# Optimization experiments

Hardware: AMD Instinct MI355X
Metric: run time of the kernel (lower is better)

Reference implementation:

```python
import jax, jax.numpy as jnp
import numpy as np

B, T, C, NH = 2, 128, 384, 6
H = 768          # memory MLP hidden (expansion=2)
P, M = 4, 16     # persistent + long-term memory tokens; prefix_len = P+M
LR, MOM, DECAY = 0.01, 0.9, 0.001

def setup_inputs() -> dict:
    key = jax.random.key(0)
    ks = jax.random.split(key, 12)
    s = 0.02
    return {
        'x':          jax.random.normal(ks[0], (B, T, C), jnp.float32),
        'c_attn_w':   jax.random.normal(ks[1], (C, 3 * C), jnp.float32) * s,
        'c_attn_b':   jnp.zeros((3 * C,), jnp.float32),
        'c_proj_w':   jax.random.normal(ks[2], (C, C), jnp.float32) * s,
        'c_proj_b':   jnp.zeros((C,), jnp.float32),
        'ln1_g': jnp.ones((C,), jnp.float32), 'ln1_b': jnp.zeros((C,), jnp.float32),
        'ln2_g': jnp.ones((C,), jnp.float32), 'ln2_b': jnp.zeros((C,), jnp.float32),
        'fc_w':       jax.random.normal(ks[3], (C, 4 * C), jnp.float32) * s,
        'fc_b':       jnp.zeros((4 * C,), jnp.float32),
        'pr_w':       jax.random.normal(ks[4], (4 * C, C), jnp.float32) * s,
        'pr_b':       jnp.zeros((C,), jnp.float32),
        'mem_w1':     jax.random.normal(ks[5], (C, H), jnp.float32) * s,
        'mem_w2':     jax.random.normal(ks[6], (H, C), jnp.float32) * s,
        'wk':         jax.random.normal(ks[7], (C, C), jnp.float32) * s,
        'wv':         jax.random.normal(ks[8], (C, C), jnp.float32) * s,
        'mem_queries': jax.random.normal(ks[9], (M, C), jnp.float32) * s,
        'persist':    jax.random.normal(ks[10], (P, C), jnp.float32) * s,
    }

def _ln(x, g, b):
    mu = jnp.mean(x, -1, keepdims=True)
    var = jnp.mean((x - mu) ** 2, -1, keepdims=True)
    return (x - mu) * jax.lax.rsqrt(var + 1e-5) * g + b

def _scan_log(gates, tokens):
    # x[t] = gate[t]*x[t-1] + token[t] via log-cumsum trick (scan axis = 1)
    while gates.ndim < tokens.ndim:
        gates = gates[..., None]
    g = jnp.clip(gates, 1e-7, 1.0 - 1e-7)
    lc = jnp.cumsum(jnp.log(g), axis=1)
    return jnp.cumsum(tokens * jnp.exp(-lc), axis=1) * jnp.exp(lc)

def _forward(x, c_attn_w, c_attn_b, c_proj_w, c_proj_b, ln1_g, ln1_b, ln2_g, ln2_b,
             fc_w, fc_b, pr_w, pr_b, mem_w1, mem_w2, wk, wv, mem_queries, persist):
    b = x.shape[0]
    hd = C // NH
    PL = P + M
    xn = _ln(x, ln1_g, ln1_b)
    # --- retrieve long-term memory tokens with previous-segment memory weights ---
    retr = jax.nn.silu(mem_queries @ mem_w1) @ mem_w2              # [M, C]
    pref = jnp.concatenate([persist, retr], axis=0)                # [PL, C]
    seq = jnp.concatenate([jnp.broadcast_to(pref, (b, PL, C)), xn], axis=1)  # [b, t, C]
    t = seq.shape[1]
    # --- prefix-LM masked attention ---
    qkv = seq @ c_attn_w + c_attn_b
    q, k, v = jnp.split(qkv, 3, axis=-1)
    def heads(z):
        return z.reshape(b, t, NH, hd).transpose(0, 2, 1, 3)       # [b, nh, t, hd]
    q, k, v = heads(q), heads(k), heads(v)
    sc = jnp.einsum('bhqd,bhkd->bhqk', q, k) / np.float32(np.sqrt(hd))
    idx = jnp.arange(t)
    kp = idx < PL  # key in prefix
    # prefix_lm_mask: key_in_prefix OR (both in suffix AND causal)
    allowed = kp[None, :] | ((~kp[:, None]) & (~kp[None, :]) & (idx[:, None] >= idx[None, :]))
    sc = jnp.where(allowed, sc, -jnp.inf)
    y = jnp.einsum('bhqk,bhkd->bhqd', jax.nn.softmax(sc, axis=-1), v)
    y = y.transpose(0, 2, 1, 3).reshape(b, t, C) @ c_proj_w + c_proj_b
    h1 = x + y[:, PL:, :]                                          # suffix (segment) outputs
    h2n = _ln(h1, ln2_g, ln2_b)
    h2 = h1 + (jax.nn.gelu(h2n @ fc_w + fc_b) @ pr_w + pr_b)
    # --- Titans neural memory update (per-token grads + momentum/decay scans) ---
    km = xn @ wk                                                   # [b, T, C]
    vm = xn @ wv
    hh = km @ mem_w1                                               # [b, T, H]
    a = jax.nn.silu(hh)
    err = a @ mem_w2 - vm                                          # [b, T, C]
    dw2 = jnp.einsum('bth,btc->bthc', a, err)                      # [b, T, H, C]
    sg = jax.nn.sigmoid(hh)
    dh = (err @ mem_w2.T) * (sg * (1.0 + hh * (1.0 - sg)))         # silu'
    dw1 = jnp.einsum('btc,bth->btch', km, dh)                      # [b, T, C, H]
    gm = jnp.full((b, T), MOM, x.dtype)
    scale = -(LR * (1.0 - MOM))
    m1 = _scan_log(gm, scale * dw1)
    m2 = _scan_log(gm, scale * dw2)
    def upd(w0, m):  # W[t] = (1-decay)*W[t-1] + m[t], W[-1] = w0
        toks = jnp.concatenate([jnp.broadcast_to(w0, (b,) + w0.shape)[:, None], m], axis=1)
        g = jnp.concatenate([jnp.ones((b, 1), x.dtype),
                             jnp.full((b, T), 1.0 - DECAY, x.dtype)], axis=1)
        return _scan_log(g, toks)[:, -1]
    w1f = upd(mem_w1, m1)                                          # [b, C, H]
    w2f = upd(mem_w2, m2)                                          # [b, H, C]
    # --- combine block output with updated-memory retrieval ---
    mem_out = jnp.einsum('bth,bhc->btc',
                         jax.nn.silu(jnp.einsum('btc,bch->bth', h2, w1f)), w2f)
    return h2 + mem_out

def reference(x, c_attn_w, c_attn_b, c_proj_w, c_proj_b, ln1_g, ln1_b, ln2_g, ln2_b,
              fc_w, fc_b, pr_w, pr_b, mem_w1, mem_w2, wk, wv, mem_queries, persist):
    return _forward(x, c_attn_w, c_attn_b, c_proj_w, c_proj_b, ln1_g, ln1_b, ln2_g, ln2_b,
                    fc_w, fc_b, pr_w, pr_b, mem_w1, mem_w2, wk, wv, mem_queries, persist)
```

## Files before the change

### kernel.cpp

```cpp
#include <hip/hip_runtime.h>
#include <math.h>

#define B_ 2
#define T_ 128
#define Cc 384
#define NH_ 6
#define HD 64
#define Hh 768
#define P_ 4
#define M_ 16
#define PL_ 20
#define TT 148

typedef unsigned short u16;
typedef short short8 __attribute__((ext_vector_type(8)));
typedef float f32x4 __attribute__((ext_vector_type(4)));

__device__ __forceinline__ u16 f2bf(float f) {
  unsigned int u = __float_as_uint(f);
  u += 0x7FFFu + ((u >> 16) & 1u);
  return (u16)(u >> 16);
}
__device__ __forceinline__ float siluf(float v) { return v / (1.f + expf(-v)); }
__device__ __forceinline__ float geluf(float v) {
  float x3 = v*v*v;
  return 0.5f*v*(1.f + tanhf(0.7978845608028654f*(v + 0.044715f*x3)));
}
template<int ACT> __device__ __forceinline__ float act_apply(float v) {
  if (ACT == 1) return geluf(v);
  if (ACT == 2) return siluf(v);
  return v;
}
__device__ __forceinline__ float coef_f(int k) {
  float e = (float)(T_ - k);
  return (exp2f(e * -0.00144342f) - exp2f(e * -0.15200310f)) * (1.0f/0.099f);
}
__device__ __forceinline__ void st_tr4(u16* dst, float v0, float v1, float v2, float v3) {
  union { u16 u[4]; uint2 d; } q;
  q.u[0]=f2bf(v0); q.u[1]=f2bf(v1); q.u[2]=f2bf(v2); q.u[3]=f2bf(v3);
  *(uint2*)dst = q.d;
}
__device__ __forceinline__ float wave_sum(float s) {
  #pragma unroll
  for (int off = 32; off; off >>= 1) s += __shfl_xor(s, off);
  return s;
}

struct Prm {
  const float *x,*c_attn_w,*c_attn_b,*c_proj_w,*c_proj_b,*ln1_g,*ln1_b,*ln2_g,*ln2_b,
              *fc_w,*fc_b,*pr_w,*pr_b,*mem_w1,*mem_w2,*wk,*wv,*mem_q,*persist;
  float *qkv,*vmb,*h1,*h2,*hhb,*outp;
  u16 *cattnT,*cprojT,*wkT,*wvT,*fcT,*prT,*w1tr,*w2tr,*w2pl,*memq,*hid,*seqb,*yb,*h2n,
      *fco,*h2b,*kmb,*kmTc,*ab,*abTc,*errB,*errT,*dhT,*w1fT,*w2fT,*ub;
  float scale, dpow;
};

template<int KSTEPS>
__device__ __forceinline__ void mfma_core(const u16* __restrict__ A,
    const u16* __restrict__ BT, int M, int mBase, int nBase, float (*red)[64][36])
{
  const long K = (long)KSTEPS * 128;
  int l = threadIdx.x & 63, w = threadIdx.x >> 6;
  int lr = l & 15, kg = l >> 4;
  long r0 = (long)min(mBase + lr, M - 1);
  long r1 = (long)min(mBase + 16 + lr, M - 1);
  long c0 = nBase + lr;
  long ko = (long)w * KSTEPS * 32 + kg * 8;
  const u16* pa0 = A + r0*K + ko;
  const u16* pa1 = A + r1*K + ko;
  const u16* pb0 = BT + c0*K + ko;
  const u16* pb1 = BT + (c0+16)*K + ko;
  const u16* pb2 = BT + (c0+32)*K + ko;
  const u16* pb3 = BT + (c0+48)*K + ko;
  f32x4 acc[2][4] = {};
  short8 a0 = *(const short8*)pa0, a1 = *(const short8*)pa1;
  short8 b0 = *(const short8*)pb0, b1 = *(const short8*)pb1;
  short8 b2 = *(const short8*)pb2, b3 = *(const short8*)pb3;
  #pragma unroll
  for (int t = 0; t < KSTEPS; ++t) {
    short8 xa0=a0, xa1=a1, xb0=b0, xb1=b1, xb2=b2, xb3=b3;
    if (t+1 < KSTEPS) {
      int o = (t+1)*32;
      a0 = *(const short8*)(pa0+o); a1 = *(const short8*)(pa1+o);
      b0 = *(const short8*)(pb0+o); b1 = *(const short8*)(pb1+o);
      b2 = *(const short8*)(pb2+o); b3 = *(const short8*)(pb3+o);
    }
    acc[0][0] = __builtin_amdgcn_mfma_f32_16x16x32_bf16(xa0, xb0, acc[0][0], 0,0,0);
    acc[0][1] = __builtin_amdgcn_mfma_f32_16x16x32_bf16(xa0, xb1, acc[0][1], 0,0,0);
    acc[0][2] = __builtin_amdgcn_mfma_f32_16x16x32_bf16(xa0, xb2, acc[0][2], 0,0,0);
    acc[0][3] = __builtin_amdgcn_mfma_f32_16x16x32_bf16(xa0, xb3, acc[0][3], 0,0,0);
    acc[1][0] = __builtin_amdgcn_mfma_f32_16x16x32_bf16(xa1, xb0, acc[1][0], 0,0,0);
    acc[1][1] = __builtin_amdgcn_mfma_f32_16x16x32_bf16(xa1, xb1, acc[1][1], 0,0,0);
    acc[1][2] = __builtin_amdgcn_mfma_f32_16x16x32_bf16(xa1, xb2, acc[1][2], 0,0,0);
    acc[1][3] = __builtin_amdgcn_mfma_f32_16x16x32_bf16(xa1, xb3, acc[1][3], 0,0,0);
  }
  #pragma unroll
  for (int i = 0; i < 2; ++i)
    #pragma unroll
    for (int j = 0; j < 4; ++j)
      *(f32x4*)&red[w][j*16 + lr][i*16 + kg*4] = acc[i][j];
  __syncthreads();
}

__device__ __forceinline__ void reduce8(float (*red)[64][36], float v[8], int& row0, int& col) {
  int tid = threadIdx.x;
  col = tid & 63;
  row0 = (tid >> 6) * 8;
  #pragma unroll
  for (int q = 0; q < 2; ++q) {
    f32x4 s = *(f32x4*)&red[0][col][row0 + q*4];
    s += *(f32x4*)&red[1][col][row0 + q*4];
    s += *(f32x4*)&red[2][col][row0 + q*4];
    s += *(f32x4*)&red[3][col][row0 + q*4];
    v[q*4+0] = s[0]; v[q*4+1] = s[1]; v[q*4+2] = s[2]; v[q*4+3] = s[3];
  }
}

template<int KSTEPS, int ACT, bool BIAS, bool RES, bool STF, bool STB, bool STTR>
__device__ __forceinline__ void gemm_task(const u16* A, const u16* BT,
    const float* bias, const float* res, float rscale,
    float* outF, u16* outB, u16* outT, int M, int N,
    int xx, int yy, float (*red)[64][36])
{
  int mBase = yy*32, nBase = xx*64;
  mfma_core<KSTEPS>(A, BT, M, mBase, nBase, red);
  float v[8]; int row0, col;
  reduce8(red, v, row0, col);
  int c = nBase + col;
  float bv = BIAS ? bias[c] : 0.f;
  #pragma unroll
  for (int q = 0; q < 8; ++q) {
    int r = mBase + row0 + q;
    float val = act_apply<ACT>(v[q] + bv);
    if (RES && r < M) val += rscale * res[(long)r*N + c];
    v[q] = val;
    if (r < M) {
      if (STF) outF[(long)r*N + c] = val;
      if (STB) outB[(long)r*N + c] = f2bf(val);
    }
  }
  if (STTR) {
    #pragma unroll
    for (int q = 0; q < 2; ++q) {
      int r = mBase + row0 + q*4;
      if (r < M) {
        int zz = r >> 7, t0 = r & 127;
        st_tr4(&outT[((long)zz*N + c)*128 + t0], v[q*4], v[q*4+1], v[q*4+2], v[q*4+3]);
      }
    }
  }
}

__global__ __launch_bounds__(256)
void k0_prep(Prm p)
{
  __shared__ float lds[1056];
  const int t = blockIdx.x;
  const int tid = threadIdx.x, w = tid >> 6, lane = tid & 63;
  if (t < 2592) {
    const float* src; u16* dst; int K, N, tile;
    int b = t;
    if (b < 432)       { src=p.c_attn_w; dst=p.cattnT; K=384;  N=1152; tile=b; }
    else if (b < 576)  { src=p.c_proj_w; dst=p.cprojT; K=384;  N=384;  tile=b-432; }
    else if (b < 720)  { src=p.wk;       dst=p.wkT;    K=384;  N=384;  tile=b-576; }
    else if (b < 864)  { src=p.wv;       dst=p.wvT;    K=384;  N=384;  tile=b-720; }
    else if (b < 1440) { src=p.fc_w;     dst=p.fcT;    K=384;  N=1536; tile=b-864; }
    else if (b < 2016) { src=p.pr_w;     dst=p.prT;    K=1536; N=384;  tile=b-1440; }
    else if (b < 2304) { src=p.mem_w1;   dst=p.w1tr;   K=384;  N=768;  tile=b-2016; }
    else               { src=p.mem_w2;   dst=p.w2tr;   K=768;  N=384;  tile=b-2304; }
    int ntx = N >> 5;
    int n0 = (tile % ntx) << 5, k0 = (tile / ntx) << 5;
    float (*fl)[33] = reinterpret_cast<float(*)[33]>(lds);
    int tr = tid >> 3, tc4 = (tid & 7) << 2;
    float4 vv = *(const float4*)&src[(long)(k0 + tr)*N + n0 + tc4];
    fl[tr][tc4] = vv.x; fl[tr][tc4+1] = vv.y; fl[tr][tc4+2] = vv.z; fl[tr][tc4+3] = vv.w;
    __syncthreads();
    st_tr4(&dst[(long)(n0 + tr)*K + k0 + tc4],
           fl[tc4][tr], fl[tc4+1][tr], fl[tc4+2][tr], fl[tc4+3][tr]);
  } else if (t < 2888) {
    int i = (t - 2592)*256 + tid;
    if (i < 73728) {
      float4 v = *(const float4*)&p.mem_w2[(long)i*4];
      st_tr4(&p.w2pl[(long)i*4], v.x, v.y, v.z, v.w);
    } else if (i < 73728 + 1536) {
      int j = i - 73728;
      float4 v = *(const float4*)&p.mem_q[(long)j*4];
      st_tr4(&p.memq[(long)j*4], v.x, v.y, v.z, v.w);
    } else if (i < 73728 + 1536 + 384) {
      int j = i - 73728 - 1536;
      float4 v = *(const float4*)&p.persist[(long)j*4];
      st_tr4(&p.seqb[(long)j*4], v.x, v.y, v.z, v.w);
      st_tr4(&p.seqb[(long)TT*384 + j*4], v.x, v.y, v.z, v.w);
    }
  } else {
    int row = (t - 2888)*4 + w;
    const float* src = p.x + (long)row*384;
    float v[6];
    #pragma unroll
    for (int i = 0; i < 6; ++i) v[i] = src[lane + i*64];
    float mu = wave_sum(v[0]+v[1]+v[2]+v[3]+v[4]+v[5]) * (1.f/384.f);
    float sq = 0.f;
    #pragma unroll
    for (int i = 0; i < 6; ++i) { float d = v[i]-mu; sq += d*d; }
    float rstd = rsqrtf(wave_sum(sq)*(1.f/384.f) + 1e-5f);
    u16* dst = p.seqb + ((long)(row >> 7)*TT + PL_ + (row & 127))*384;
    #pragma unroll
    for (int i = 0; i < 6; ++i) {
      int cc = lane + i*64;
      dst[cc] = f2bf((v[i]-mu)*rstd*p.ln1_g[cc] + p.ln1_b[cc]);
    }
  }
}

__global__ __launch_bounds__(256, 2)
void k0b_hid(Prm p)
{
  __shared__ float red[4][64][36];
  gemm_task<3,2,false,false,false,true,false>(p.memq, p.w1tr, nullptr, nullptr, 0.f,
      nullptr, p.hid, nullptr, 16, 768, blockIdx.x, 0, red);
}

__global__ __launch_bounds__(256, 2)
void k0c_retr(Prm p)
{
  __shared__ float red[4][64][36];
  int nBase = blockIdx.x*64;
  mfma_core<6>(p.hid, p.w2tr, 16, 0, nBase, red);
  float v[8]; int row0, col;
  reduce8(red, v, row0, col);
  int c = nBase + col;
  #pragma unroll
  for (int q = 0; q < 8; ++q) {
    int r = row0 + q;
    if (r < 16) {
      u16 bv = f2bf(v[q]);
      p.seqb[(long)(P_ + r)*384 + c] = bv;
      p.seqb[(long)(TT + P_ + r)*384 + c] = bv;
    }
  }
}

__global__ __launch_bounds__(256, 2)
void k1_qkv(Prm p)
{
  __shared__ float red[4][64][36];
  int t = blockIdx.x;
  int xx = t % 30, yy = t / 30;
  int nb = xx * 64;
  const u16* BT; int n0, seg;
  if (nb < 1152)      { BT = p.cattnT; n0 = nb;        seg = 0; }
  else if (nb < 1536) { BT = p.wkT;    n0 = nb - 1152; seg = 1; }
  else                { BT = p.wvT;    n0 = nb - 1536; seg = 2; }
  int mBase = yy*32;
  mfma_core<3>(p.seqb, BT, 296, mBase, n0, red);
  float v[8]; int row0, col;
  reduce8(red, v, row0, col);
  int c = n0 + col;
  if (seg == 0) {
    float bv = p.c_attn_b[c];
    #pragma unroll
    for (int q = 0; q < 8; ++q) {
      int r = mBase + row0 + q;
      if (r < 296) p.qkv[(long)r*1152 + c] = v[q] + bv;
    }
  } else if (seg == 1) {
    #pragma unroll
    for (int q = 0; q < 8; ++q) {
      int r = mBase + row0 + q;
      if (r < 296) {
        int z = r/148, tt2 = r - 20 - z*148;
        if (tt2 >= 0) p.kmb[((long)z*128 + tt2)*384 + c] = f2bf(v[q]);
      }
    }
    #pragma unroll
    for (int q = 0; q < 2; ++q) {
      int r = mBase + row0 + q*4;
      if (r < 296) {
        int z = r/148, t0 = r - 20 - z*148;
        if (t0 >= 0)
          st_tr4(&p.kmTc[((long)z*384 + c)*128 + t0],
                 v[q*4]*coef_f(t0), v[q*4+1]*coef_f(t0+1),
                 v[q*4+2]*coef_f(t0+2), v[q*4+3]*coef_f(t0+3));
      }
    }
  } else {
    #pragma unroll
    for (int q = 0; q < 8; ++q) {
      int r = mBase + row0 + q;
      if (r < 296) {
        int z = r/148, tt2 = r - 20 - z*148;
        if (tt2 >= 0) p.vmb[((long)z*128 + tt2)*384 + c] = v[q];
      }
    }
  }
}

__global__ __launch_bounds__(256, 2)
void k2_attn_hh(Prm p)
{
  __shared__ float red[4][64][36];
  const int t = blockIdx.x;
  const int tid = threadIdx.x, w = tid >> 6, lane = tid & 63;
  if (t < 384) {
    float* ldsf = (float*)red;
    float* qs = ldsf + w*64;
    float* pp = ldsf + 256 + w*152;
    int tt = t*4 + w;
    int qr = PL_ + (tt & 127);
    int h  = (tt >> 7) % 6;
    int b  = (tt / 768) & 1;
    const float* base = p.qkv + (long)b*TT*1152;
    qs[lane] = base[(long)qr*1152 + h*64 + lane];
    float mloc = -1e30f;
    for (int k = lane; k < TT; k += 64) {
      float s = -1e30f;
      if (k <= qr) {
        const float* kp = base + (long)k*1152 + 384 + h*64;
        float acc = 0.f;
        #pragma unroll
        for (int d = 0; d < 64; ++d) acc += qs[d]*kp[d];
        s = acc * 0.125f;
      }
      pp[k] = s;
      mloc = fmaxf(mloc, s);
    }
    #pragma unroll
    for (int off = 32; off; off >>= 1) mloc = fmaxf(mloc, __shfl_xor(mloc, off));
    float ssum = 0.f;
    for (int k = lane; k < TT; k += 64) {
      float e = (k <= qr) ? expf(pp[k] - mloc) : 0.f;
      pp[k] = e; ssum += e;
    }
    ssum = wave_sum(ssum);
    float inv = 1.f / ssum;
    float acc = 0.f;
    const float* vb = base + 768 + h*64 + lane;
    int k = 0;
    for (; k + 4 <= qr + 1; k += 4)
      acc += pp[k]*vb[(long)k*1152] + pp[k+1]*vb[(long)(k+1)*1152]
           + pp[k+2]*vb[(long)(k+2)*1152] + pp[k+3]*vb[(long)(k+3)*1152];
    for (; k <= qr; ++k) acc += pp[k]*vb[(long)k*1152];
    p.yb[((long)b*128 + (tt & 127))*384 + h*64 + lane] = f2bf(acc * inv);
  } else {
    int tt2 = t - 384;
    int xx = tt2 % 12, yy = tt2 / 12;
    int mBase = yy*32, nBase = xx*64;
    mfma_core<3>(p.kmb, p.w1tr, 256, mBase, nBase, red);
    float v[8]; int row0, col;
    reduce8(red, v, row0, col);
    int c = nBase + col;
    float s8[8];
    #pragma unroll
    for (int q = 0; q < 8; ++q) {
      int r = mBase + row0 + q;
      p.hhb[(long)r*768 + c] = v[q];
      s8[q] = siluf(v[q]);
      p.ab[(long)r*768 + c] = f2bf(s8[q]);
    }
    #pragma unroll
    for (int q = 0; q < 2; ++q) {
      int r = mBase + row0 + q*4;
      int zz = r >> 7, t0 = r & 127;
      st_tr4(&p.abTc[((long)zz*768 + c)*128 + t0],
             s8[q*4]*coef_f(t0), s8[q*4+1]*coef_f(t0+1),
             s8[q*4+2]*coef_f(t0+2), s8[q*4+3]*coef_f(t0+3));
    }
  }
}

__global__ __launch_bounds__(256, 2)
void k3_h1err(Prm p)
{
  __shared__ float red[4][64][36];
  int t = blockIdx.x;
  if (t < 48) {
    gemm_task<3,0,true,true,true,false,false>(p.yb, p.cprojT, p.c_proj_b, p.x, 1.f,
        p.h1, nullptr, nullptr, 256, 384, t % 6, t / 6, red);
  } else {
    int tt2 = t - 48;
    gemm_task<6,0,false,true,false,true,true>(p.ab, p.w2tr, nullptr, p.vmb, -1.f,
        nullptr, p.errB, p.errT, 256, 384, tt2 % 6, tt2 / 6, red);
  }
}

__global__ __launch_bounds__(256, 2)
void k4_ln2dh(Prm p)
{
  __shared__ float red[4][64][36];
  int t = blockIdx.x;
  const int tid = threadIdx.x, w = tid >> 6, lane = tid & 63;
  if (t < 64) {
    int row = t*4 + w;
    const float* src = p.h1 + (long)row*384;
    float v[6];
    #pragma unroll
    for (int i = 0; i < 6; ++i) v[i] = src[lane + i*64];
    float mu = wave_sum(v[0]+v[1]+v[2]+v[3]+v[4]+v[5]) * (1.f/384.f);
    float sq = 0.f;
    #pragma unroll
    for (int i = 0; i < 6; ++i) { float d = v[i]-mu; sq += d*d; }
    float rstd = rsqrtf(wave_sum(sq)*(1.f/384.f) + 1e-5f);
    u16* dst = p.h2n + (long)row*384;
    #pragma unroll
    for (int i = 0; i < 6; ++i) {
      int cc = lane + i*64;
      dst[cc] = f2bf((v[i]-mu)*rstd*p.ln2_g[cc] + p.ln2_b[cc]);
    }
  } else {
    int tt2 = t - 64;
    int xx = tt2 % 12, yy = tt2 / 12;
    int mBase = yy*32, nBase = xx*64;
    mfma_core<3>(p.errB, p.w2pl, 256, mBase, nBase, red);
    float v[8]; int row0, col;
    reduce8(red, v, row0, col);
    int c = nBase + col;
    #pragma unroll
    for (int q = 0; q < 8; ++q) {
      int r = mBase + row0 + q;
      float h = p.hhb[(long)r*768 + c];
      float sg = 1.f/(1.f + expf(-h));
      v[q] = v[q] * (sg*(1.f + h*(1.f - sg)));
    }
    #pragma unroll
    for (int q = 0; q < 2; ++q) {
      int r = mBase + row0 + q*4;
      int zz = r >> 7, t0 = r & 127;
      st_tr4(&p.dhT[((long)zz*768 + c)*128 + t0], v[q*4], v[q*4+1], v[q*4+2], v[q*4+3]);
    }
  }
}

__global__ __launch_bounds__(256, 2)
void k5_fcowupd(Prm p)
{
  __shared__ float red[4][64][36];
  int t = blockIdx.x;
  if (t < 192) {
    gemm_task<3,1,true,false,false,true,false>(p.h2n, p.fcT, p.fc_b, nullptr, 0.f,
        nullptr, p.fco, nullptr, 256, 1536, t % 24, t / 24, red);
  } else {
    const u16 *A, *BT; const float* W0; u16* Oz; int M, N, xx, yy, z;
    if (t < 480) {
      int tt2 = t - 192;
      xx = tt2 % 12; yy = (tt2 / 12) % 12; z = tt2 / 144;
      M = 384; N = 768;
      A = p.kmTc + (long)z*M*128; BT = p.dhT + (long)z*N*128;
      W0 = p.mem_w1; Oz = p.w1fT + (long)z*M*N;
    } else {
      int tt2 = t - 480;
      xx = tt2 % 6; yy = (tt2 / 6) % 24; z = tt2 / 144;
      M = 768; N = 384;
      A = p.abTc + (long)z*M*128; BT = p.errT + (long)z*N*128;
      W0 = p.mem_w2; Oz = p.w2fT + (long)z*M*N;
    }
    int mBase = yy*32, nBase = xx*64;
    mfma_core<1>(A, BT, M, mBase, nBase, red);
    float v[8]; int row0, col;
    reduce8(red, v, row0, col);
    int c = nBase + col;
    #pragma unroll
    for (int q = 0; q < 8; ++q) {
      int r = mBase + row0 + q;
      v[q] = p.dpow*W0[(long)r*N + c] + p.scale*v[q];
    }
    int r0 = mBase + row0;
    st_tr4(&Oz[(long)c*M + r0],     v[0], v[1], v[2], v[3]);
    st_tr4(&Oz[(long)c*M + r0 + 4], v[4], v[5], v[6], v[7]);
  }
}

__global__ __launch_bounds__(256, 2)
void k6_h2(Prm p)
{
  __shared__ float red[4][64][36];
  int t = blockIdx.x;
  gemm_task<12,0,true,true,true,true,false>(p.fco, p.prT, p.pr_b, p.h1, 1.f,
      p.h2, p.h2b, nullptr, 256, 384, t % 6, t / 6, red);
}

__global__ __launch_bounds__(256, 2)
void k7_ub(Prm p)
{
  __shared__ float red[4][64][36];
  int t = blockIdx.x;
  int z = t / 48, rr = t % 48;
  gemm_task<3,2,false,false,false,true,false>(
      p.h2b + (long)z*128*384, p.w1fT + (long)z*768*384, nullptr, nullptr, 0.f,
      nullptr, p.ub + (long)z*128*768, nullptr, 128, 768, rr % 12, rr / 12, red);
}

__global__ __launch_bounds__(256, 2)
void k8_out(Prm p)
{
  __shared__ float red[4][64][36];
  int t = blockIdx.x;
  int z = t / 24, rr = t % 24;
  gemm_task<6,0,false,true,true,false,false>(
      p.ub + (long)z*128*768, p.w2fT + (long)z*384*768, nullptr,
      p.h2 + (long)z*128*384, 1.f,
      p.outp + (long)z*128*384, nullptr, nullptr, 128, 384, rr % 6, rr / 6, red);
}

extern "C" void kernel_launch(void* const* d_in, const int* in_sizes, int n_in,
                              void* d_out, int out_size, void* d_ws, size_t ws_size,
                              hipStream_t stream)
{
  Prm p;
  p.x        = (const float*)d_in[0];
  p.c_attn_w = (const float*)d_in[1];
  p.c_attn_b = (const float*)d_in[2];
  p.c_proj_w = (const float*)d_in[3];
  p.c_proj_b = (const float*)d_in[4];
  p.ln1_g    = (const float*)d_in[5];
  p.ln1_b    = (const float*)d_in[6];
  p.ln2_g    = (const float*)d_in[7];
  p.ln2_b    = (const float*)d_in[8];
  p.fc_w     = (const float*)d_in[9];
  p.fc_b     = (const float*)d_in[10];
  p.pr_w     = (const float*)d_in[11];
  p.pr_b     = (const float*)d_in[12];
  p.mem_w1   = (const float*)d_in[13];
  p.mem_w2   = (const float*)d_in[14];
  p.wk       = (const float*)d_in[15];
  p.wv       = (const float*)d_in[16];
  p.mem_q    = (const float*)d_in[17];
  p.persist  = (const float*)d_in[18];

  float* f = (float*)d_ws;
  p.qkv = f;            f += 296L*1152;
  p.vmb = f;            f += 256L*384;
  p.h1  = f;            f += 256L*384;
  p.h2  = f;            f += 256L*384;
  p.hhb = f;            f += 256L*768;
  u16* b = (u16*)f;
  p.cattnT = b;  b += 1152L*384;
  p.cprojT = b;  b += 384L*384;
  p.wkT    = b;  b += 384L*384;
  p.wvT    = b;  b += 384L*384;
  p.fcT    = b;  b += 1536L*384;
  p.prT    = b;  b += 384L*1536;
  p.w1tr   = b;  b += 768L*384;
  p.w2tr   = b;  b += 384L*768;
  p.w2pl   = b;  b += 768L*384;
  p.memq   = b;  b += 16L*384;
  p.hid    = b;  b += 16L*768;
  p.seqb   = b;  b += 2L*TT*384;
  p.yb     = b;  b += 256L*384;
  p.h2n    = b;  b += 256L*384;
  p.fco    = b;  b += 256L*1536;
  p.h2b    = b;  b += 256L*384;
  p.kmb    = b;  b += 256L*384;
  p.kmTc   = b;  b += 2L*384*128;
  p.ab     = b;  b += 256L*768;
  p.abTc   = b;  b += 2L*768*128;
  p.errB   = b;  b += 256L*384;
  p.errT   = b;  b += 2L*384*128;
  p.dhT    = b;  b += 2L*768*128;
  p.w1fT   = b;  b += 2L*768*384;
  p.w2fT   = b;  b += 2L*384*768;
  p.ub     = b;  b += 2L*128*768;
  p.outp   = (float*)d_out;
  p.dpow   = powf(0.999f, 128.f);
  p.scale  = -0.001f;

  hipLaunchKernelGGL(k0_prep,    dim3(2952), dim3(256), 0, stream, p);
  hipLaunchKernelGGL(k0b_hid,    dim3(12),   dim3(256), 0, stream, p);
  hipLaunchKernelGGL(k0c_retr,   dim3(6),    dim3(256), 0, stream, p);
  hipLaunchKernelGGL(k1_qkv,     dim3(300),  dim3(256), 0, stream, p);
  hipLaunchKernelGGL(k2_attn_hh, dim3(480),  dim3(256), 0, stream, p);
  hipLaunchKernelGGL(k3_h1err,   dim3(96),   dim3(256), 0, stream, p);
  hipLaunchKernelGGL(k4_ln2dh,   dim3(160),  dim3(256), 0, stream, p);
  hipLaunchKernelGGL(k5_fcowupd, dim3(768),  dim3(256), 0, stream, p);
  hipLaunchKernelGGL(k6_h2,      dim3(48),   dim3(256), 0, stream, p);
  hipLaunchKernelGGL(k7_ub,      dim3(96),   dim3(256), 0, stream, p);
  hipLaunchKernelGGL(k8_out,     dim3(48),   dim3(256), 0, stream, p);
}
```

Before: 92.62 us.

## Fold memory-query hidden GEMM into prep kernel, widen transpose tiles, stage attention K/V in LDS

The separate k0b_hid launch is removed. The memory-query hidden projection is now computed with silu directly from fp32 weights inside the prep kernel, which also drops the bf16 memq staging buffer. Weight transposes move from 32x32 to 64x64 LDS tiles, so the prep grid has far fewer blocks. The attention path now loads K and V rows for a head cooperatively into LDS once per block and shares them across its four waves, replacing per-lane strided global reads. In exchange it adds block-wide barriers and makes the hid GEMM a scalar FMA loop.

```diff
diff --git a/kernel.cpp b/kernel.cpp
--- a/kernel.cpp
+++ b/kernel.cpp
@@ -50,7 +50,7 @@
   const float *x,*c_attn_w,*c_attn_b,*c_proj_w,*c_proj_b,*ln1_g,*ln1_b,*ln2_g,*ln2_b,
               *fc_w,*fc_b,*pr_w,*pr_b,*mem_w1,*mem_w2,*wk,*wv,*mem_q,*persist;
   float *qkv,*vmb,*h1,*h2,*hhb,*outp;
-  u16 *cattnT,*cprojT,*wkT,*wvT,*fcT,*prT,*w1tr,*w2tr,*w2pl,*memq,*hid,*seqb,*yb,*h2n,
+  u16 *cattnT,*cprojT,*wkT,*wvT,*fcT,*prT,*w1tr,*w2tr,*w2pl,*hid,*seqb,*yb,*h2n,
       *fco,*h2b,*kmb,*kmTc,*ab,*abTc,*errB,*errT,*dhT,*w1fT,*w2fT,*ub;
   float scale, dpow;
 };
@@ -154,46 +154,50 @@
 __global__ __launch_bounds__(256)
 void k0_prep(Prm p)
 {
-  __shared__ float lds[1056];
+  __shared__ float lds[6144];
   const int t = blockIdx.x;
   const int tid = threadIdx.x, w = tid >> 6, lane = tid & 63;
-  if (t < 2592) {
+  if (t < 648) {
     const float* src; u16* dst; int K, N, tile;
     int b = t;
-    if (b < 432)       { src=p.c_attn_w; dst=p.cattnT; K=384;  N=1152; tile=b; }
-    else if (b < 576)  { src=p.c_proj_w; dst=p.cprojT; K=384;  N=384;  tile=b-432; }
-    else if (b < 720)  { src=p.wk;       dst=p.wkT;    K=384;  N=384;  tile=b-576; }
-    else if (b < 864)  { src=p.wv;       dst=p.wvT;    K=384;  N=384;  tile=b-720; }
-    else if (b < 1440) { src=p.fc_w;     dst=p.fcT;    K=384;  N=1536; tile=b-864; }
-    else if (b < 2016) { src=p.pr_w;     dst=p.prT;    K=1536; N=384;  tile=b-1440; }
-    else if (b < 2304) { src=p.mem_w1;   dst=p.w1tr;   K=384;  N=768;  tile=b-2016; }
-    else               { src=p.mem_w2;   dst=p.w2tr;   K=768;  N=384;  tile=b-2304; }
-    int ntx = N >> 5;
-    int n0 = (tile % ntx) << 5, k0 = (tile / ntx) << 5;
-    float (*fl)[33] = reinterpret_cast<float(*)[33]>(lds);
-    int tr = tid >> 3, tc4 = (tid & 7) << 2;
-    float4 vv = *(const float4*)&src[(long)(k0 + tr)*N + n0 + tc4];
-    fl[tr][tc4] = vv.x; fl[tr][tc4+1] = vv.y; fl[tr][tc4+2] = vv.z; fl[tr][tc4+3] = vv.w;
+    if (b < 108)      { src=p.c_attn_w; dst=p.cattnT; K=384;  N=1152; tile=b; }
+    else if (b < 144) { src=p.c_proj_w; dst=p.cprojT; K=384;  N=384;  tile=b-108; }
+    else if (b < 180) { src=p.wk;       dst=p.wkT;    K=384;  N=384;  tile=b-144; }
+    else if (b < 216) { src=p.wv;       dst=p.wvT;    K=384;  N=384;  tile=b-180; }
+    else if (b < 360) { src=p.fc_w;     dst=p.fcT;    K=384;  N=1536; tile=b-216; }
+    else if (b < 504) { src=p.pr_w;     dst=p.prT;    K=1536; N=384;  tile=b-360; }
+    else if (b < 576) { src=p.mem_w1;   dst=p.w1tr;   K=384;  N=768;  tile=b-504; }
+    else              { src=p.mem_w2;   dst=p.w2tr;   K=768;  N=384;  tile=b-576; }
+    int ntx = N >> 6;
+    int n0 = (tile % ntx) << 6, k0 = (tile / ntx) << 6;
+    float (*fl)[65] = reinterpret_cast<float(*)[65]>(lds);
+    int rr = tid >> 4, c4 = (tid & 15) << 2;
+    #pragma unroll
+    for (int i = 0; i < 4; ++i) {
+      int row = rr + i*16;
+      float4 vv = *(const float4*)&src[(long)(k0 + row)*N + n0 + c4];
+      fl[row][c4] = vv.x; fl[row][c4+1] = vv.y; fl[row][c4+2] = vv.z; fl[row][c4+3] = vv.w;
+    }
     __syncthreads();
-    st_tr4(&dst[(long)(n0 + tr)*K + k0 + tc4],
-           fl[tc4][tr], fl[tc4+1][tr], fl[tc4+2][tr], fl[tc4+3][tr]);
-  } else if (t < 2888) {
-    int i = (t - 2592)*256 + tid;
+    #pragma unroll
+    for (int i = 0; i < 4; ++i) {
+      int nrow = rr + i*16;
+      st_tr4(&dst[(long)(n0 + nrow)*K + k0 + c4],
+             fl[c4][nrow], fl[c4+1][nrow], fl[c4+2][nrow], fl[c4+3][nrow]);
+    }
+  } else if (t < 938) {
+    int i = (t - 648)*256 + tid;
     if (i < 73728) {
       float4 v = *(const float4*)&p.mem_w2[(long)i*4];
       st_tr4(&p.w2pl[(long)i*4], v.x, v.y, v.z, v.w);
-    } else if (i < 73728 + 1536) {
+    } else if (i < 73728 + 384) {
       int j = i - 73728;
-      float4 v = *(const float4*)&p.mem_q[(long)j*4];
-      st_tr4(&p.memq[(long)j*4], v.x, v.y, v.z, v.w);
-    } else if (i < 73728 + 1536 + 384) {
-      int j = i - 73728 - 1536;
       float4 v = *(const float4*)&p.persist[(long)j*4];
       st_tr4(&p.seqb[(long)j*4], v.x, v.y, v.z, v.w);
       st_tr4(&p.seqb[(long)TT*384 + j*4], v.x, v.y, v.z, v.w);
     }
-  } else {
-    int row = (t - 2888)*4 + w;
+  } else if (t < 1002) {
+    int row = (t - 938)*4 + w;
     const float* src = p.x + (long)row*384;
     float v[6];
     #pragma unroll
@@ -209,15 +213,29 @@
       int cc = lane + i*64;
       dst[cc] = f2bf((v[i]-mu)*rstd*p.ln1_g[cc] + p.ln1_b[cc]);
     }
-  }
-}
-
-__global__ __launch_bounds__(256, 2)
-void k0b_hid(Prm p)
-{
-  __shared__ float red[4][64][36];
-  gemm_task<3,2,false,false,false,true,false>(p.memq, p.w1tr, nullptr, nullptr, 0.f,
-      nullptr, p.hid, nullptr, 16, 768, blockIdx.x, 0, red);
+  } else {
+    for (int i = tid; i < 1536; i += 256)
+      *(float4*)&lds[i*4] = *(const float4*)&p.mem_q[(long)i*4];
+    __syncthreads();
+    int cb = t - 1002;
+    int c = cb*64 + (tid & 63);
+    int rg = (tid >> 6) * 4;
+    const float* m0 = lds + (long)rg*384;
+    const float* m1 = m0 + 384;
+    const float* m2 = m1 + 384;
+    const float* m3 = m2 + 384;
+    const float* w1c = p.mem_w1 + c;
+    float a0 = 0.f, a1 = 0.f, a2 = 0.f, a3 = 0.f;
+    #pragma unroll 8
+    for (int k = 0; k < 384; ++k) {
+      float wv2 = w1c[(long)k*768];
+      a0 += m0[k]*wv2; a1 += m1[k]*wv2; a2 += m2[k]*wv2; a3 += m3[k]*wv2;
+    }
+    p.hid[(long)(rg+0)*768 + c] = f2bf(siluf(a0));
+    p.hid[(long)(rg+1)*768 + c] = f2bf(siluf(a1));
+    p.hid[(long)(rg+2)*768 + c] = f2bf(siluf(a2));
+    p.hid[(long)(rg+3)*768 + c] = f2bf(siluf(a3));
+  }
 }
 
 __global__ __launch_bounds__(256, 2)
@@ -305,6 +323,7 @@
     float* ldsf = (float*)red;
     float* qs = ldsf + w*64;
     float* pp = ldsf + 256 + w*152;
+    float (*kv)[65] = (float(*)[65])(ldsf + 864);
     int tt = t*4 + w;
     int qr = PL_ + (tt & 127);
     int h  = (tt >> 7) % 6;
@@ -312,16 +331,24 @@
     const float* base = p.qkv + (long)b*TT*1152;
     qs[lane] = base[(long)qr*1152 + h*64 + lane];
     float mloc = -1e30f;
-    for (int k = lane; k < TT; k += 64) {
+    for (int kb = 0; kb < 3; ++kb) {
+      int k0 = kb*64;
+      int rows = (k0 + 64 <= TT) ? 64 : (TT - k0);
+      __syncthreads();
+      for (int i = tid; i < rows*16; i += 256) {
+        int row = i >> 4, c4 = (i & 15) << 2;
+        *(float4*)&kv[row][c4] = *(const float4*)&base[(long)(k0+row)*1152 + 384 + h*64 + c4];
+      }
+      __syncthreads();
+      int k = k0 + lane;
       float s = -1e30f;
-      if (k <= qr) {
-        const float* kp = base + (long)k*1152 + 384 + h*64;
+      if (k < TT && k <= qr) {
         float acc = 0.f;
         #pragma unroll
-        for (int d = 0; d < 64; ++d) acc += qs[d]*kp[d];
+        for (int d = 0; d < 64; ++d) acc += qs[d]*kv[lane][d];
         s = acc * 0.125f;
       }
-      pp[k] = s;
+      if (k < TT) pp[k] = s;
       mloc = fmaxf(mloc, s);
     }
     #pragma unroll
@@ -332,15 +359,21 @@
       pp[k] = e; ssum += e;
     }
     ssum = wave_sum(ssum);
-    float inv = 1.f / ssum;
     float acc = 0.f;
-    const float* vb = base + 768 + h*64 + lane;
-    int k = 0;
-    for (; k + 4 <= qr + 1; k += 4)
-      acc += pp[k]*vb[(long)k*1152] + pp[k+1]*vb[(long)(k+1)*1152]
-           + pp[k+2]*vb[(long)(k+2)*1152] + pp[k+3]*vb[(long)(k+3)*1152];
-    for (; k <= qr; ++k) acc += pp[k]*vb[(long)k*1152];
-    p.yb[((long)b*128 + (tt & 127))*384 + h*64 + lane] = f2bf(acc * inv);
+    for (int kb = 0; kb < 3; ++kb) {
+      int k0 = kb*64;
+      int rows = (k0 + 64 <= TT) ? 64 : (TT - k0);
+      __syncthreads();
+      for (int i = tid; i < rows*16; i += 256) {
+        int row = i >> 4, c4 = (i & 15) << 2;
+        *(float4*)&kv[row][c4] = *(const float4*)&base[(long)(k0+row)*1152 + 768 + h*64 + c4];
+      }
+      __syncthreads();
+      int jmax = qr - k0 + 1;
+      if (jmax > rows) jmax = rows;
+      for (int j = 0; j < jmax; ++j) acc += pp[k0+j]*kv[j][lane];
+    }
+    p.yb[((long)b*128 + (tt & 127))*384 + h*64 + lane] = f2bf(acc / ssum);
   } else {
     int tt2 = t - 384;
     int xx = tt2 % 12, yy = tt2 / 12;
@@ -542,7 +575,6 @@
   p.w1tr   = b;  b += 768L*384;
   p.w2tr   = b;  b += 384L*768;
   p.w2pl   = b;  b += 768L*384;
-  p.memq   = b;  b += 16L*384;
   p.hid    = b;  b += 16L*768;
   p.seqb   = b;  b += 2L*TT*384;
   p.yb     = b;  b += 256L*384;
@@ -563,8 +595,7 @@
   p.dpow   = powf(0.999f, 128.f);
   p.scale  = -0.001f;
 
-  hipLaunchKernelGGL(k0_prep,    dim3(2952), dim3(256), 0, stream, p);
-  hipLaunchKernelGGL(k0b_hid,    dim3(12),   dim3(256), 0, stream, p);
+  hipLaunchKernelGGL(k0_prep,    dim3(1014), dim3(256), 0, stream, p);
   hipLaunchKernelGGL(k0c_retr,   dim3(6),    dim3(256), 0, stream, p);
   hipLaunchKernelGGL(k1_qkv,     dim3(300),  dim3(256), 0, stream, p);
   hipLaunchKernelGGL(k2_attn_hh, dim3(480),  dim3(256), 0, stream, p);
```

Measured after the change: 103.1 us. +11.4%, slower.
